# Optimization experiments

Measured on AMD Instinct MI355X. Metric: run time of the kernel, lower is better.

The kernel has to match this reference:

```python
import jax, jax.numpy as jnp
import numpy as np
from jax import lax

DN = ('NCHW', 'OIHW', 'NCHW')

def conv(x, w, b, stride, pad):
    y = lax.conv_general_dilated(x, w, (stride, stride), [(pad, pad), (pad, pad)], dimension_numbers=DN)
    return y + b[None, :, None, None]

def setup_inputs() -> dict:
    key = jax.random.key(0)
    ks = jax.random.split(key, 16)
    s = 0.05
    inp = {
        'condition': jax.random.normal(ks[0], (16, 1, 256, 256), jnp.float32),
        'w1': jax.random.normal(ks[1], (64, 1, 4, 4), jnp.float32) * s,
        'b1': jnp.zeros((64,), jnp.float32),
        'w2': jax.random.normal(ks[2], (128, 64, 4, 4), jnp.float32) * s,
        'b2': jnp.zeros((128,), jnp.float32),
        'w3': jax.random.normal(ks[3], (128, 128, 3, 3), jnp.float32) * s,
        'b3': jnp.zeros((128,), jnp.float32),
        'r1w1': jax.random.normal(ks[4], (32, 128, 3, 3), jnp.float32) * s,
        'r1b1': jnp.zeros((32,), jnp.float32),
        'r1w2': jax.random.normal(ks[5], (128, 32, 1, 1), jnp.float32) * s,
        'r1b2': jnp.zeros((128,), jnp.float32),
        'r2w1': jax.random.normal(ks[6], (32, 128, 3, 3), jnp.float32) * s,
        'r2b1': jnp.zeros((32,), jnp.float32),
        'r2w2': jax.random.normal(ks[7], (128, 32, 1, 1), jnp.float32) * s,
        'r2b2': jnp.zeros((128,), jnp.float32),
        'wpre': jax.random.normal(ks[8], (4, 128, 1, 1), jnp.float32) * s,
        'bpre': jnp.zeros((4,), jnp.float32),
        'codebook': jax.random.normal(ks[9], (2048, 4), jnp.float32),
    }
    return inp

def reference(condition, w1, b1, w2, b2, w3, b3, r1w1, r1b1, r1w2, r1b2,
              r2w1, r2b1, r2w2, r2b2, wpre, bpre, codebook):
    # --- conv encoder (VQ-VAE standard) ---
    h = jax.nn.relu(conv(condition, w1, b1, 2, 1))   # [B,64,128,128]
    h = jax.nn.relu(conv(h, w2, b2, 2, 1))           # [B,128,64,64]
    h = conv(h, w3, b3, 1, 1)                        # [B,128,64,64]
    # residual stack: 2 blocks of relu->3x3->relu->1x1, residual add
    for wa, ba, wb, bb in ((r1w1, r1b1, r1w2, r1b2), (r2w1, r2b1, r2w2, r2b2)):
        t = conv(jax.nn.relu(h), wa, ba, 1, 1)
        t = conv(jax.nn.relu(t), wb, bb, 1, 0)
        h = h + t
    h = jax.nn.relu(h)
    z = conv(h, wpre, bpre, 1, 0)                    # [B,4,64,64]
    # --- cosine-distance vector quantization ---
    B, D, H, W = z.shape
    zf = jnp.transpose(z, (0, 2, 3, 1)).reshape(-1, D)          # [BHW, D]
    zn = zf / (jnp.linalg.norm(zf, axis=-1, keepdims=True) + 1e-12)
    en = codebook / (jnp.linalg.norm(codebook, axis=-1, keepdims=True) + 1e-12)
    sim = jnp.einsum('nd,kd->nk', zn, en)                       # cosine similarity
    idx = jnp.argmax(sim, axis=-1)                              # nearest code
    q = codebook[idx].reshape(B, H, W, D)
    c = jnp.transpose(q, (0, 3, 1, 2))                          # [B,4,64,64]
    return c
```

## Files before the change

### kernel.cpp

```cpp
#include <hip/hip_runtime.h>
#include <math.h>


typedef short v8s __attribute__((ext_vector_type(8)));
typedef float v4f __attribute__((ext_vector_type(4)));

#define B_OFF 4194304
#define A_OFF 12582912
#define W2_S 0
#define W3_S 393216
#define WR1_S 835584
#define WR2_S 946176
#define WP1_S 1056768
#define WP2_S 1069056

__device__ inline void limb3(float v, unsigned short& h, unsigned short& m,
                             unsigned short& l) {
    unsigned ub = __float_as_uint(v);
    unsigned hb = ub & 0xffff0000u;
    float r1 = v - __uint_as_float(hb);
    unsigned mb = __float_as_uint(r1) & 0xffff0000u;
    float r2 = r1 - __uint_as_float(mb);
    unsigned lb = __float_as_uint(r2) & 0xffff0000u;
    h = (unsigned short)(hb >> 16);
    m = (unsigned short)(mb >> 16);
    l = (unsigned short)(lb >> 16);
}

struct CfgConv2 {
    static constexpr int NC = 8, NT = 4, OC = 128;
    static constexpr bool RELU_IN = false, RELU_OUT = true;
    __device__ static void tap(int c, int t, int& ry, int& rx) {
        int py = (c >> 2) & 1, px = (c >> 1) & 1;
        ry = (t >> 1) - py; rx = (t & 1) - px;
    }
    __device__ static bool gaddr(int n, int oy, int r, int X, int icp, int c,
                                 int& g0, int& g1) {
        int py = (c >> 2) & 1, px = (c >> 1) & 1;
        int Yg = 2 * (oy + r - 1) + py;
        if (Yg < 0 || Yg >= 128) return false;
        int pi = (c & 1) * 16 + icp;
        g0 = ((n * 128 + Yg) * 32 + pi) * 256 + 2 * X + px;
        g1 = g0 + 128;
        return true;
    }
    __device__ static int widx(int c, int t, int oc, int ic) {
        int py = (c >> 2) & 1, px = (c >> 1) & 1, half = c & 1;
        int dy = 2 * (t >> 1) + (1 - py), dx = 2 * (t & 1) + (1 - px);
        return ((oc * 64 + half * 32 + ic) * 4 + dy) * 4 + dx;
    }
};
struct CfgConv3 {
    static constexpr int NC = 4, NT = 9, OC = 128;
    static constexpr bool RELU_IN = false, RELU_OUT = false;
    __device__ static void tap(int c, int t, int& ry, int& rx) {
        ry = t / 3 - 1; rx = t % 3 - 1;
    }
    __device__ static bool gaddr(int n, int oy, int r, int X, int icp, int c,
                                 int& g0, int& g1) {
        int Yg = oy + r - 1;
        if (Yg < 0 || Yg >= 64) return false;
        int pi = c * 16 + icp;
        g0 = ((n * 64 + Yg) * 64 + pi) * 128 + X;
        g1 = g0 + 64;
        return true;
    }
    __device__ static int widx(int c, int t, int oc, int ic) {
        return ((oc * 128 + c * 32 + ic) * 3 + t / 3) * 3 + t % 3;
    }
};
struct CfgRes {
    static constexpr int NC = 4, NT = 9, OC = 32;
    __device__ static int widx(int c, int t, int oc, int ic) {
        return ((oc * 128 + c * 32 + ic) * 3 + t / 3) * 3 + t % 3;
    }
};
struct Cfg1x1 {
    static constexpr int NC = 1, NT = 1, OC = 128;
    __device__ static int widx(int c, int t, int oc, int ic) {
        return oc * 32 + ic;
    }
};

template <typename C>
__device__ inline void repack_one(const float* __restrict__ w,
                                  short* __restrict__ dst, int idx) {
    int s  = idx & 31;
    int oc = (idx >> 5) % C::OC;
    int ct = idx / (32 * C::OC);
    int c = ct / C::NT, t = ct % C::NT;
    float val = w[C::widx(c, t, oc, s)];
    unsigned short h, m, l;
    limb3(val, h, m, l);
    constexpr int NTILE = C::OC / 16;
    int nt = oc >> 4, o = oc & 15, q = s >> 3, j = s & 7;
    int fr = ((q * 16 + o) << 3) + j;
    dst[(((ct * 3 + 0) * NTILE + nt) << 9) + fr] = (short)h;
    dst[(((ct * 3 + 1) * NTILE + nt) << 9) + fr] = (short)m;
    dst[(((ct * 3 + 2) * NTILE + nt) << 9) + fr] = (short)l;
}

__global__ __launch_bounds__(256) void repack_all_k(
    const float* __restrict__ w2, const float* __restrict__ w3,
    const float* __restrict__ r1, const float* __restrict__ r2,
    const float* __restrict__ p1, const float* __restrict__ p2,
    short* __restrict__ base)
{
    int idx = blockIdx.x * 256 + threadIdx.x;
    if (idx < 131072) { repack_one<CfgConv2>(w2, base + W2_S, idx); return; }
    idx -= 131072;
    if (idx < 147456) { repack_one<CfgConv3>(w3, base + W3_S, idx); return; }
    idx -= 147456;
    if (idx < 36864)  { repack_one<CfgRes>(r1, base + WR1_S, idx); return; }
    idx -= 36864;
    if (idx < 36864)  { repack_one<CfgRes>(r2, base + WR2_S, idx); return; }
    idx -= 36864;
    if (idx < 4096)   { repack_one<Cfg1x1>(p1, base + WP1_S, idx); return; }
    idx -= 4096;
    if (idx < 4096)   { repack_one<Cfg1x1>(p2, base + WP2_S, idx); }
}

template <typename C>
__global__ __launch_bounds__(256, 3) void mfma_conv(
    const float* __restrict__ in, const short* __restrict__ repw,
    const float* __restrict__ bias, float* __restrict__ out, int n0)
{
    constexpr int APLANE = 3 * 66 * 32;
    constexpr int NTILE  = C::OC / 16;
    __shared__ __align__(16) short lA[3 * APLANE];

    int tid = threadIdx.x;
    int lane = tid & 63, wv = tid >> 6;
    int n_img = blockIdx.x >> 6, oy = blockIdx.x & 63;

    for (int idx = tid; idx < 3 * 3 * 2 * 16; idx += 256) {
        int plane = idx / 96;
        int rem = idx % 96;
        int rr = rem / 32;
        int hc = (rem / 16) & 1;
        int d = idx & 15;
        ((unsigned*)lA)[plane * 3168 + (rr * 66 + hc * 65) * 16 + d] = 0;
    }

    v4f acc[4][2] = {};
    int nbase = wv * 2;
    int Xq = tid & 15, icp = tid >> 4, quad = lane >> 4;

    float pv[24];
    auto issue_loads = [&](int c) {
#pragma unroll
        for (int it = 0; it < 12; it++) {
            int r = it >> 2, xg = it & 3;
            int X = xg * 16 + Xq;
            int g0, g1;
            float v0 = 0.f, v1 = 0.f;
            if (C::gaddr(n_img, oy, r, X, icp, c, g0, g1)) {
                v0 = in[g0];
                v1 = in[g1];
            }
            pv[2 * it] = v0; pv[2 * it + 1] = v1;
        }
    };
    auto load_bf = [&](int c, int t, v8s (&dst)[2][3]) {
#pragma unroll
        for (int nt = 0; nt < 2; nt++)
#pragma unroll
            for (int L = 0; L < 3; L++)
                dst[nt][L] = *(const v8s*)(repw +
                    ((((c * C::NT + t) * 3 + L) * NTILE + (nbase + nt)) << 9) +
                    (lane << 3));
    };

    issue_loads(0);

    for (int c = 0; c < C::NC; c++) {
        __syncthreads();
#pragma unroll
        for (int it = 0; it < 12; it++) {
            int r = it >> 2, xg = it & 3;
            int X = xg * 16 + Xq;
            float v0 = pv[2 * it], v1 = pv[2 * it + 1];
            if constexpr (C::RELU_IN) { v0 = fmaxf(v0, 0.f); v1 = fmaxf(v1, 0.f); }
            unsigned short h0, m0, l0, h1, m1, l1;
            limb3(v0, h0, m0, l0);
            limb3(v1, m1, m1, l1);
            limb3(v1, h1, m1, l1);
            int cell = r * 66 + X + 1;
            int f = (cell + (cell >> 2)) & 3;
            int phys = (icp & 3) + 4 * (((icp >> 2) + f) & 3);
            unsigned* pa = (unsigned*)lA + cell * 16 + phys;
            pa[0]        = (unsigned)h0 | ((unsigned)h1 << 16);
            pa[3168]     = (unsigned)m0 | ((unsigned)m1 << 16);
            pa[2 * 3168] = (unsigned)l0 | ((unsigned)l1 << 16);
        }
        __syncthreads();
        if (c + 1 < C::NC) issue_loads(c + 1);

        v8s bf[2][2][3];
        load_bf(c, 0, bf[0]);
#pragma unroll
        for (int t = 0; t < C::NT; t++) {
            constexpr int NTT = C::NT;
            if (t + 1 < NTT) load_bf(c, t + 1, bf[(t + 1) & 1]);
            int ry, rx;
            C::tap(c, t, ry, rx);
#pragma unroll
            for (int mt = 0; mt < 4; mt++) {
                int x = mt * 16 + (lane & 15);
                int cell = (ry + 1) * 66 + (x + rx + 1);
                int f = (cell + (cell >> 2)) & 3;
                int aa = cell * 32 + (((quad + f) & 3) << 3);
                v8s ah = *(const v8s*)&lA[aa];
                v8s am = *(const v8s*)&lA[APLANE + aa];
                v8s al = *(const v8s*)&lA[2 * APLANE + aa];
#pragma unroll
                for (int nt = 0; nt < 2; nt++) {
                    v4f a0 = acc[mt][nt];
                    a0 = __builtin_amdgcn_mfma_f32_16x16x32_bf16(ah, bf[t & 1][nt][0], a0, 0, 0, 0);
                    a0 = __builtin_amdgcn_mfma_f32_16x16x32_bf16(ah, bf[t & 1][nt][1], a0, 0, 0, 0);
                    a0 = __builtin_amdgcn_mfma_f32_16x16x32_bf16(am, bf[t & 1][nt][0], a0, 0, 0, 0);
                    a0 = __builtin_amdgcn_mfma_f32_16x16x32_bf16(am, bf[t & 1][nt][1], a0, 0, 0, 0);
                    a0 = __builtin_amdgcn_mfma_f32_16x16x32_bf16(ah, bf[t & 1][nt][2], a0, 0, 0, 0);
                    a0 = __builtin_amdgcn_mfma_f32_16x16x32_bf16(al, bf[t & 1][nt][0], a0, 0, 0, 0);
                    acc[mt][nt] = a0;
                }
            }
        }
    }
#pragma unroll
    for (int mt = 0; mt < 4; mt++) {
        int x0 = mt * 16 + quad * 4;
#pragma unroll
        for (int nt = 0; nt < 2; nt++) {
            int oc = (nbase + nt) * 16 + (lane & 15);
            float bv = bias[oc];
            float v0 = acc[mt][nt][0] + bv;
            float v1 = acc[mt][nt][1] + bv;
            float v2 = acc[mt][nt][2] + bv;
            float v3 = acc[mt][nt][3] + bv;
            if constexpr (C::RELU_OUT) {
                v0 = fmaxf(v0, 0.f); v1 = fmaxf(v1, 0.f);
                v2 = fmaxf(v2, 0.f); v3 = fmaxf(v3, 0.f);
            }
            float4 o = make_float4(v0, v1, v2, v3);
            int off = (((n0 + n_img) * 64 + oy) * 64 + (oc >> 1)) * 128 +
                      (oc & 1) * 64 + x0;
            *(float4*)&out[off] = o;
        }
    }
}

__global__ __launch_bounds__(256) void mfma_res(
    const float* __restrict__ in, const short* __restrict__ repw,
    const float* __restrict__ b1, const short* __restrict__ repp,
    const float* __restrict__ b2, float* __restrict__ out)
{
    constexpr int PLANE_D = 4 * 66 * 16;
    constexpr int PLANE_S = 2 * PLANE_D;
    __shared__ __align__(16) short lA[3 * PLANE_S];

    int tid = threadIdx.x;
    int lane = tid & 63, wv = tid >> 6;
    int n_img = blockIdx.x >> 5;
    int oy0 = (blockIdx.x & 31) << 1;
    int jrow = wv >> 1, xh = wv & 1;

    for (int idx = tid; idx < 3 * 4 * 2 * 16; idx += 256) {
        int plane = idx / 128;
        int rem = idx % 128;
        int rr = rem / 32;
        int hc = (rem >> 4) & 1;
        int d = idx & 15;
        ((unsigned*)lA)[plane * PLANE_D + (rr * 66 + hc * 65) * 16 + d] = 0;
    }

    v4f acc[2][2] = {};
    int Xq = tid & 15, icp = tid >> 4, quad = lane >> 4;

    float pv[32];
    auto issue_loads = [&](int c) {
#pragma unroll
        for (int it = 0; it < 16; it++) {
            int r = it >> 2, xg = it & 3;
            int X = xg * 16 + Xq;
            int Yg = oy0 + r - 1;
            float v0 = 0.f, v1 = 0.f;
            if (Yg >= 0 && Yg < 64) {
                int g = ((n_img * 64 + Yg) * 64 + (c * 16 + icp)) * 128 + X;
                v0 = in[g];
                v1 = in[g + 64];
            }
            pv[2 * it] = v0; pv[2 * it + 1] = v1;
        }
    };

    issue_loads(0);

    for (int c = 0; c < 4; c++) {
        __syncthreads();
#pragma unroll
        for (int it = 0; it < 16; it++) {
            int r = it >> 2, xg = it & 3;
            int X = xg * 16 + Xq;
            float v0 = fmaxf(pv[2 * it], 0.f);
            float v1 = fmaxf(pv[2 * it + 1], 0.f);
            unsigned short h0, m0, l0, h1, m1, l1;
            limb3(v0, h0, m0, l0);
            limb3(v1, h1, m1, l1);
            int cell = r * 66 + X + 1;
            int f = (cell + (cell >> 2)) & 3;
            int phys = (icp & 3) + 4 * (((icp >> 2) + f) & 3);
            unsigned* pa = (unsigned*)lA + cell * 16 + phys;
            pa[0]           = (unsigned)h0 | ((unsigned)h1 << 16);
            pa[PLANE_D]     = (unsigned)m0 | ((unsigned)m1 << 16);
            pa[2 * PLANE_D] = (unsigned)l0 | ((unsigned)l1 << 16);
        }
        __syncthreads();
        if (c + 1 < 4) issue_loads(c + 1);

        v8s bf[2][2][3];
        auto load_bf = [&](int t, v8s (&dst)[2][3]) {
#pragma unroll
            for (int nt = 0; nt < 2; nt++)
#pragma unroll
                for (int L = 0; L < 3; L++)
                    dst[nt][L] = *(const v8s*)(repw +
                        ((((c * 9 + t) * 3 + L) * 2 + nt) << 9) + (lane << 3));
        };
        load_bf(0, bf[0]);
#pragma unroll
        for (int t = 0; t < 9; t++) {
            if (t + 1 < 9) load_bf(t + 1, bf[(t + 1) & 1]);
            int ry = t / 3 - 1, rx = t % 3 - 1;
#pragma unroll
            for (int mti = 0; mti < 2; mti++) {
                int x = (xh * 2 + mti) * 16 + (lane & 15);
                int cell = (jrow + ry + 1) * 66 + (x + rx + 1);
                int f = (cell + (cell >> 2)) & 3;
                int aa = cell * 32 + (((quad + f) & 3) << 3);
                v8s ah = *(const v8s*)&lA[aa];
                v8s am = *(const v8s*)&lA[PLANE_S + aa];
                v8s al = *(const v8s*)&lA[2 * PLANE_S + aa];
#pragma unroll
                for (int nt = 0; nt < 2; nt++) {
                    v4f a0 = acc[mti][nt];
                    a0 = __builtin_amdgcn_mfma_f32_16x16x32_bf16(ah, bf[t & 1][nt][0], a0, 0, 0, 0);
                    a0 = __builtin_amdgcn_mfma_f32_16x16x32_bf16(ah, bf[t & 1][nt][1], a0, 0, 0, 0);
                    a0 = __builtin_amdgcn_mfma_f32_16x16x32_bf16(am, bf[t & 1][nt][0], a0, 0, 0, 0);
                    a0 = __builtin_amdgcn_mfma_f32_16x16x32_bf16(am, bf[t & 1][nt][1], a0, 0, 0, 0);
                    a0 = __builtin_amdgcn_mfma_f32_16x16x32_bf16(ah, bf[t & 1][nt][2], a0, 0, 0, 0);
                    a0 = __builtin_amdgcn_mfma_f32_16x16x32_bf16(al, bf[t & 1][nt][0], a0, 0, 0, 0);
                    acc[mti][nt] = a0;
                }
            }
        }
    }

    __syncthreads();
#pragma unroll
    for (int mti = 0; mti < 2; mti++) {
#pragma unroll
        for (int nt = 0; nt < 2; nt++) {
            int ic = nt * 16 + (lane & 15);
            int icp2 = ic >> 1, hilo = ic & 1;
            float bv = b1[ic];
#pragma unroll
            for (int r = 0; r < 4; r++) {
                int x = (xh * 2 + mti) * 16 + quad * 4 + r;
                float v = fmaxf(acc[mti][nt][r] + bv, 0.f);
                unsigned short h, m, l;
                limb3(v, h, m, l);
                int f = (x + (x >> 2)) & 3;
                int phys = (icp2 & 3) + 4 * (((icp2 >> 2) + f) & 3);
                int sa = x * 32 + phys * 2 + hilo;
                lA[jrow * 6144 + sa]        = (short)h;
                lA[jrow * 6144 + 2048 + sa] = (short)m;
                lA[jrow * 6144 + 4096 + sa] = (short)l;
            }
        }
    }
    __syncthreads();

#pragma unroll
    for (int j = 0; j < 2; j++) {
        v4f a2[8] = {};
        int x = wv * 16 + (lane & 15);
        int f = (x + (x >> 2)) & 3;
        int aa = x * 32 + (((quad + f) & 3) << 3);
        v8s ah = *(const v8s*)&lA[j * 6144 + aa];
        v8s am = *(const v8s*)&lA[j * 6144 + 2048 + aa];
        v8s al = *(const v8s*)&lA[j * 6144 + 4096 + aa];
#pragma unroll
        for (int nt = 0; nt < 8; nt++) {
            v8s bh = *(const v8s*)(repp + ((0 * 8 + nt) << 9) + (lane << 3));
            v8s bm = *(const v8s*)(repp + ((1 * 8 + nt) << 9) + (lane << 3));
            v8s bl = *(const v8s*)(repp + ((2 * 8 + nt) << 9) + (lane << 3));
            v4f a0 = a2[nt];
            a0 = __builtin_amdgcn_mfma_f32_16x16x32_bf16(ah, bh, a0, 0, 0, 0);
            a0 = __builtin_amdgcn_mfma_f32_16x16x32_bf16(ah, bm, a0, 0, 0, 0);
            a0 = __builtin_amdgcn_mfma_f32_16x16x32_bf16(am, bh, a0, 0, 0, 0);
            a0 = __builtin_amdgcn_mfma_f32_16x16x32_bf16(am, bm, a0, 0, 0, 0);
            a0 = __builtin_amdgcn_mfma_f32_16x16x32_bf16(ah, bl, a0, 0, 0, 0);
            a0 = __builtin_amdgcn_mfma_f32_16x16x32_bf16(al, bh, a0, 0, 0, 0);
            a2[nt] = a0;
        }
#pragma unroll
        for (int nt = 0; nt < 8; nt++) {
            int oc = nt * 16 + (lane & 15);
            int x0 = wv * 16 + quad * 4;
            int off = ((n_img * 64 + (oy0 + j)) * 64 + (oc >> 1)) * 128 +
                      (oc & 1) * 64 + x0;
            float4 hv = *(const float4*)&in[off];
            float bv = b2[oc];
            float4 o = make_float4(hv.x + a2[nt][0] + bv, hv.y + a2[nt][1] + bv,
                                   hv.z + a2[nt][2] + bv, hv.w + a2[nt][3] + bv);
            *(float4*)&out[off] = o;
        }
    }
}

__global__ __launch_bounds__(256) void conv1_k(
    const float* __restrict__ x, const float* __restrict__ w,
    const float* __restrict__ b, float* __restrict__ out)
{
    int tid = blockIdx.x * 256 + threadIdx.x;
    int n   = tid >> 14;
    int rem = tid & 16383;
    int oy  = rem >> 7;
    int ox  = rem & 127;
    int iy0 = oy * 2 - 1, ix0 = ox * 2 - 1;
    const float* xb = x + n * 65536;
    float v[16];
#pragma unroll
    for (int ky = 0; ky < 4; ky++) {
#pragma unroll
        for (int kx = 0; kx < 4; kx++) {
            int iy = iy0 + ky, ix = ix0 + kx;
            bool ok = (iy >= 0) & (iy < 256) & (ix >= 0) & (ix < 256);
            v[ky * 4 + kx] = ok ? xb[iy * 256 + ix] : 0.f;
        }
    }
    int obase = (n * 128 + oy) * 8192 + ox;
    for (int oc = 0; oc < 64; oc++) {
        float acc = b[oc];
        const float* wp = w + oc * 16;
#pragma unroll
        for (int k = 0; k < 16; k++) acc = fmaf(v[k], wp[k], acc);
        out[obase + (oc >> 1) * 256 + (oc & 1) * 128] = fmaxf(acc, 0.f);
    }
}

__global__ __launch_bounds__(256) void prevq_k(
    const float* __restrict__ h, const float* __restrict__ wpre,
    const float* __restrict__ bpre, const float* __restrict__ cb,
    float* __restrict__ out)
{
    __shared__ float4 en[2048];
    for (int i = threadIdx.x; i < 2048; i += 256) {
        float c0 = cb[i * 4 + 0], c1 = cb[i * 4 + 1];
        float c2 = cb[i * 4 + 2], c3 = cb[i * 4 + 3];
        float nrm = sqrtf(c0 * c0 + c1 * c1 + c2 * c2 + c3 * c3) + 1e-12f;
        en[i] = make_float4(c0 / nrm, c1 / nrm, c2 / nrm, c3 / nrm);
    }
    __syncthreads();

    int tid = blockIdx.x * 256 + threadIdx.x;
    int n   = tid >> 12;
    int pos = tid & 4095;
    int y = pos >> 6, xx = pos & 63;
    const float* hb = h + ((n * 64 + y) * 64) * 128 + xx;
    float z0 = bpre[0], z1 = bpre[1], z2 = bpre[2], z3 = bpre[3];
    for (int icp = 0; icp < 64; icp++) {
        float v0 = fmaxf(hb[icp * 128], 0.f);
        int ic = 2 * icp;
        z0 = fmaf(v0, wpre[ic],       z0);
        z1 = fmaf(v0, wpre[128 + ic], z1);
        z2 = fmaf(v0, wpre[256 + ic], z2);
        z3 = fmaf(v0, wpre[384 + ic], z3);
        float v1 = fmaxf(hb[icp * 128 + 64], 0.f);
        z0 = fmaf(v1, wpre[ic + 1],       z0);
        z1 = fmaf(v1, wpre[128 + ic + 1], z1);
        z2 = fmaf(v1, wpre[256 + ic + 1], z2);
        z3 = fmaf(v1, wpre[384 + ic + 1], z3);
    }
    float best = -1e30f;
    int   bidx = 0;
    for (int k = 0; k < 2048; k++) {
        float4 e = en[k];
        float s = z0 * e.x + z1 * e.y + z2 * e.z + z3 * e.w;
        if (s > best) { best = s; bidx = k; }
    }
    const float* q = cb + bidx * 4;
    out[(n * 4 + 0) * 4096 + pos] = q[0];
    out[(n * 4 + 1) * 4096 + pos] = q[1];
    out[(n * 4 + 2) * 4096 + pos] = q[2];
    out[(n * 4 + 3) * 4096 + pos] = q[3];
}

extern "C" void kernel_launch(void* const* d_in, const int* in_sizes, int n_in,
                              void* d_out, int out_size, void* d_ws, size_t ws_size,
                              hipStream_t stream)
{
    const float* x    = (const float*)d_in[0];
    const float* w1   = (const float*)d_in[1];
    const float* b1   = (const float*)d_in[2];
    const float* w2   = (const float*)d_in[3];
    const float* b2   = (const float*)d_in[4];
    const float* w3   = (const float*)d_in[5];
    const float* b3   = (const float*)d_in[6];
    const float* r1w1 = (const float*)d_in[7];
    const float* r1b1 = (const float*)d_in[8];
    const float* r1w2 = (const float*)d_in[9];
    const float* r1b2 = (const float*)d_in[10];
    const float* r2w1 = (const float*)d_in[11];
    const float* r2b1 = (const float*)d_in[12];
    const float* r2w2 = (const float*)d_in[13];
    const float* r2b2 = (const float*)d_in[14];
    const float* wpre = (const float*)d_in[15];
    const float* bpre = (const float*)d_in[16];
    const float* cb   = (const float*)d_in[17];
    float* out = (float*)d_out;

    float* ws   = (float*)d_ws;
    short* wsS  = (short*)d_ws;
    float* B = ws + B_OFF;
    float* A = ws + A_OFF;

    repack_all_k<<<1408, 256, 0, stream>>>(w2, w3, r1w1, r2w1, r1w2, r2w2, wsS);

    conv1_k<<<512, 256, 0, stream>>>(x,               w1, b1, A);
    mfma_conv<CfgConv2><<<512, 256, 0, stream>>>(A, wsS + W2_S, b2, B, 0);
    conv1_k<<<512, 256, 0, stream>>>(x + 8 * 65536,   w1, b1, A);
    mfma_conv<CfgConv2><<<512, 256, 0, stream>>>(A, wsS + W2_S, b2, B, 8);

    mfma_conv<CfgConv3><<<1024, 256, 0, stream>>>(B, wsS + W3_S, b3, A, 0);

    mfma_res<<<512, 256, 0, stream>>>(A, wsS + WR1_S, r1b1, wsS + WP1_S, r1b2, B);
    mfma_res<<<512, 256, 0, stream>>>(B, wsS + WR2_S, r2b1, wsS + WP2_S, r2b2, A);

    prevq_k<<<256, 256, 0, stream>>>(A, wpre, bpre, cb, out);
}
```

Measured before the change: 462.3 us.

## Parallelize VQ argmax across threads and phase-split conv1 output layout

The pre-VQ kernel now splits the 128-channel 1x1 projection across four waves, combining the partial sums in shared memory. Each pixel's 2048-entry codebook argmax is split across four lanes and merged with xor shuffles, using a lowest-index tie-break. The launch grows to 1024 blocks so more threads share the serial scan. Conv1 writes a (py,px) phase-split layout so the stride-2 conv2 gathers contiguous rows. A redundant limb split is also dropped. In exchange, the codebook is normalised four times as often across blocks, and there is an extra shared-memory reduction step.

After: 456.6 us. No clear change (-1.2%).

```diff
diff --git a/kernel.cpp b/kernel.cpp
--- a/kernel.cpp
+++ b/kernel.cpp
@@ -37,11 +37,11 @@
     __device__ static bool gaddr(int n, int oy, int r, int X, int icp, int c,
                                  int& g0, int& g1) {
         int py = (c >> 2) & 1, px = (c >> 1) & 1;
-        int Yg = 2 * (oy + r - 1) + py;
-        if (Yg < 0 || Yg >= 128) return false;
+        int y2 = oy + r - 1;
+        if (y2 < 0 || y2 >= 64) return false;
         int pi = (c & 1) * 16 + icp;
-        g0 = ((n * 128 + Yg) * 32 + pi) * 256 + 2 * X + px;
-        g1 = g0 + 128;
+        g0 = (((n * 4 + py * 2 + px) * 64 + y2) * 32 + pi) * 128 + X;
+        g1 = g0 + 64;
         return true;
     }
     __device__ static int widx(int c, int t, int oc, int ic) {
@@ -183,7 +183,6 @@
             if constexpr (C::RELU_IN) { v0 = fmaxf(v0, 0.f); v1 = fmaxf(v1, 0.f); }
             unsigned short h0, m0, l0, h1, m1, l1;
             limb3(v0, h0, m0, l0);
-            limb3(v1, m1, m1, l1);
             limb3(v1, h1, m1, l1);
             int cell = r * 66 + X + 1;
             int f = (cell + (cell >> 2)) & 3;
@@ -440,13 +439,14 @@
             v[ky * 4 + kx] = ok ? xb[iy * 256 + ix] : 0.f;
         }
     }
-    int obase = (n * 128 + oy) * 8192 + ox;
+    int py = oy & 1, y2 = oy >> 1, px = ox & 1, x2 = ox >> 1;
+    int obase = (((n * 4 + py * 2 + px) * 64 + y2) * 32) * 128 + x2;
     for (int oc = 0; oc < 64; oc++) {
         float acc = b[oc];
         const float* wp = w + oc * 16;
 #pragma unroll
         for (int k = 0; k < 16; k++) acc = fmaf(v[k], wp[k], acc);
-        out[obase + (oc >> 1) * 256 + (oc & 1) * 128] = fmaxf(acc, 0.f);
+        out[obase + (oc >> 1) * 128 + (oc & 1) * 64] = fmaxf(acc, 0.f);
     }
 }
 
@@ -456,45 +456,63 @@
     float* __restrict__ out)
 {
     __shared__ float4 en[2048];
+    __shared__ float4 zpart[4][64];
     for (int i = threadIdx.x; i < 2048; i += 256) {
         float c0 = cb[i * 4 + 0], c1 = cb[i * 4 + 1];
         float c2 = cb[i * 4 + 2], c3 = cb[i * 4 + 3];
         float nrm = sqrtf(c0 * c0 + c1 * c1 + c2 * c2 + c3 * c3) + 1e-12f;
         en[i] = make_float4(c0 / nrm, c1 / nrm, c2 / nrm, c3 / nrm);
     }
+
+    int t = threadIdx.x;
+    {
+        int w = t >> 6, pl = t & 63;
+        int gpos = blockIdx.x * 64 + pl;
+        int n = gpos >> 12, pos = gpos & 4095;
+        int y = pos >> 6, xx = pos & 63;
+        const float* hb = h + ((n * 64 + y) * 64) * 128 + xx;
+        float z0 = 0.f, z1 = 0.f, z2 = 0.f, z3 = 0.f;
+        for (int icp = w * 16; icp < w * 16 + 16; icp++) {
+            float v0 = fmaxf(hb[icp * 128], 0.f);
+            int ic = 2 * icp;
+            z0 = fmaf(v0, wpre[ic],       z0);
+            z1 = fmaf(v0, wpre[128 + ic], z1);
+            z2 = fmaf(v0, wpre[256 + ic], z2);
+            z3 = fmaf(v0, wpre[384 + ic], z3);
+            float v1 = fmaxf(hb[icp * 128 + 64], 0.f);
+            z0 = fmaf(v1, wpre[ic + 1],       z0);
+            z1 = fmaf(v1, wpre[128 + ic + 1], z1);
+            z2 = fmaf(v1, wpre[256 + ic + 1], z2);
+            z3 = fmaf(v1, wpre[384 + ic + 1], z3);
+        }
+        zpart[w][pl] = make_float4(z0, z1, z2, z3);
+    }
     __syncthreads();
 
-    int tid = blockIdx.x * 256 + threadIdx.x;
-    int n   = tid >> 12;
-    int pos = tid & 4095;
-    int y = pos >> 6, xx = pos & 63;
-    const float* hb = h + ((n * 64 + y) * 64) * 128 + xx;
-    float z0 = bpre[0], z1 = bpre[1], z2 = bpre[2], z3 = bpre[3];
-    for (int icp = 0; icp < 64; icp++) {
-        float v0 = fmaxf(hb[icp * 128], 0.f);
-        int ic = 2 * icp;
-        z0 = fmaf(v0, wpre[ic],       z0);
-        z1 = fmaf(v0, wpre[128 + ic], z1);
-        z2 = fmaf(v0, wpre[256 + ic], z2);
-        z3 = fmaf(v0, wpre[384 + ic], z3);
-        float v1 = fmaxf(hb[icp * 128 + 64], 0.f);
-        z0 = fmaf(v1, wpre[ic + 1],       z0);
-        z1 = fmaf(v1, wpre[128 + ic + 1], z1);
-        z2 = fmaf(v1, wpre[256 + ic + 1], z2);
-        z3 = fmaf(v1, wpre[384 + ic + 1], z3);
-    }
+    int part = t & 3, pl = t >> 2;
+    int gpos = blockIdx.x * 64 + pl;
+    int n = gpos >> 12, pos = gpos & 4095;
+    float4 p0 = zpart[0][pl], p1 = zpart[1][pl];
+    float4 p2 = zpart[2][pl], p3 = zpart[3][pl];
+    float z0 = bpre[0] + p0.x + p1.x + p2.x + p3.x;
+    float z1 = bpre[1] + p0.y + p1.y + p2.y + p3.y;
+    float z2 = bpre[2] + p0.z + p1.z + p2.z + p3.z;
+    float z3 = bpre[3] + p0.w + p1.w + p2.w + p3.w;
+
     float best = -1e30f;
-    int   bidx = 0;
-    for (int k = 0; k < 2048; k++) {
+    int   bidx = part * 512;
+    for (int k = part * 512; k < part * 512 + 512; k++) {
         float4 e = en[k];
         float s = z0 * e.x + z1 * e.y + z2 * e.z + z3 * e.w;
         if (s > best) { best = s; bidx = k; }
     }
-    const float* q = cb + bidx * 4;
-    out[(n * 4 + 0) * 4096 + pos] = q[0];
-    out[(n * 4 + 1) * 4096 + pos] = q[1];
-    out[(n * 4 + 2) * 4096 + pos] = q[2];
-    out[(n * 4 + 3) * 4096 + pos] = q[3];
+#pragma unroll
+    for (int d = 1; d < 4; d <<= 1) {
+        float ob = __shfl_xor(best, d);
+        int   oi = __shfl_xor(bidx, d);
+        if (ob > best || (ob == best && oi < bidx)) { best = ob; bidx = oi; }
+    }
+    out[(n * 4 + part) * 4096 + pos] = cb[bidx * 4 + part];
 }
 
 extern "C" void kernel_launch(void* const* d_in, const int* in_sizes, int n_in,
@@ -538,5 +556,5 @@
     mfma_res<<<512, 256, 0, stream>>>(A, wsS + WR1_S, r1b1, wsS + WP1_S, r1b2, B);
     mfma_res<<<512, 256, 0, stream>>>(B, wsS + WR2_S, r2b1, wsS + WP2_S, r2b2, A);
 
-    prevq_k<<<256, 256, 0, stream>>>(A, wpre, bpre, cb, out);
-}
+    prevq_k<<<1024, 256, 0, stream>>>(A, wpre, bpre, cb, out);
+}
```
